# Kernel tuning notes

Hardware: AMD Instinct MI355X
Metric: run time of the kernel (lower is better)

## Reference

```python
import jax, jax.numpy as jnp
import numpy as np

N_UNI = 32; N_G = 4; N_PPG = 8
MAX_D = 100.0; MIN_D = 0.5
SOM_SIGMA = 2.0; G_STD = 2.5
ORIG = jnp.array([-25.6, -25.6, -2.0], jnp.float32); VS = 0.4
NZ = 16; GW = 128; GL = 128; DIM = 128
H_IMG = 352; W_IMG = 1216

def pe(x):
    # positional encoding: num_freqs=6, include_input -> 3 + 36 = 39 dims
    f = 2.0 ** jnp.arange(6, dtype=x.dtype)
    xf = x[..., None] * f  # (...,3,6)
    s = x.shape[:-1]
    return jnp.concatenate([x, jnp.sin(xf).reshape(s + (18,)), jnp.cos(xf).reshape(s + (18,))], axis=-1)

def resnet_fc(z, x, P):
    # pixelNeRF-style ResnetFC with latent injection per block
    w_in, b_in, wz, bz, w0, b0, w1, b1, w_out, b_out = P
    h = x @ w_in + b_in
    for i in range(3):
        h = h + z @ wz[i] + bz[i]
        net = jax.nn.relu(h) @ w0[i] + b0[i]
        h = h + jax.nn.relu(net) @ w1[i] + b1[i]
    return jax.nn.relu(h) @ w_out + b_out

def trilinear(grid, pts):
    # grid: (NZ,GW,GL,DIM); pts: (N,3) lidar coords -> trilinear gather, 0 outside
    g = (pts - ORIG) / VS
    gx, gy, gz = g[:, 0], g[:, 1], g[:, 2]
    inb = (gx >= 0) & (gx <= GW - 1) & (gy >= 0) & (gy <= GL - 1) & (gz >= 0) & (gz <= NZ - 1)
    gx = jnp.clip(gx, 0.0, GW - 1.0); gy = jnp.clip(gy, 0.0, GL - 1.0); gz = jnp.clip(gz, 0.0, NZ - 1.0)
    x0 = jnp.clip(jnp.floor(gx).astype(jnp.int32), 0, GW - 2)
    y0 = jnp.clip(jnp.floor(gy).astype(jnp.int32), 0, GL - 2)
    z0 = jnp.clip(jnp.floor(gz).astype(jnp.int32), 0, NZ - 2)
    fx = gx - x0; fy = gy - y0; fz = gz - z0
    def c(zi, xi, yi, w):
        return grid[zi, xi, yi] * w[:, None]
    feat = (c(z0, x0, y0, (1 - fz) * (1 - fx) * (1 - fy)) + c(z0, x0, y0 + 1, (1 - fz) * (1 - fx) * fy)
            + c(z0, x0 + 1, y0, (1 - fz) * fx * (1 - fy)) + c(z0, x0 + 1, y0 + 1, (1 - fz) * fx * fy)
            + c(z0 + 1, x0, y0, fz * (1 - fx) * (1 - fy)) + c(z0 + 1, x0, y0 + 1, fz * (1 - fx) * fy)
            + c(z0 + 1, x0 + 1, y0, fz * fx * (1 - fy)) + c(z0 + 1, x0 + 1, y0 + 1, fz * fx * fy))
    return feat * inb[:, None].astype(feat.dtype)

def bilinear(img, uv):
    # img: (3,H,W); uv: (N,2) (u=col, v=row) -> (N,3)
    _, H, W = img.shape
    u = jnp.clip(uv[:, 0], 0.0, W - 1.0); v = jnp.clip(uv[:, 1], 0.0, H - 1.0)
    u0 = jnp.clip(jnp.floor(u).astype(jnp.int32), 0, W - 2)
    v0 = jnp.clip(jnp.floor(v).astype(jnp.int32), 0, H - 2)
    fu = u - u0; fv = v - v0
    g = lambda vi, ui: img[:, vi, ui]
    out = (g(v0, u0) * ((1 - fv) * (1 - fu)) + g(v0, u0 + 1) * ((1 - fv) * fu)
           + g(v0 + 1, u0) * (fv * (1 - fu)) + g(v0 + 1, u0 + 1) * (fv * fu))
    return out.T

def _forward(bev_feature, cam_K, img_source, img_target, T_source2infer, T_source2target,
             gaussian_noise, Pm, Pg, sampled_pixels):
    R = sampled_pixels.shape[0]
    # (B, C, W, L) -> (n_z, W, L, dim)
    vf = bev_feature[0].reshape(NZ, DIM, GW, GL).transpose(0, 2, 3, 1)
    inv_K = jnp.linalg.inv(cam_K)
    pix = sampled_pixels.astype(jnp.float32)
    homog = jnp.concatenate([pix, jnp.ones((R, 1), jnp.float32)], axis=1)
    dirs = homog @ inv_K.T
    unit = dirs / jnp.linalg.norm(dirs, axis=1, keepdims=True)  # (R,3) cam frame
    Rsi = T_source2infer[:3, :3]; tsi = T_source2infer[:3, 3]
    viewdir = unit @ Rsi.T  # lidar frame

    # --- predict per-ray gaussian means/stds at coarse segment centers ---
    base = (jnp.arange(N_G, dtype=jnp.float32) + 0.5) * (MAX_D / N_G)
    pg = (unit[:, None, :] * base[None, :, None]).reshape(-1, 3) @ Rsi.T + tsi
    fg = trilinear(vf, pg)
    vdg = jnp.broadcast_to(viewdir[:, None, :], (R, N_G, 3)).reshape(-1, 3)
    og = resnet_fc(fg, jnp.concatenate([pe(pg), vdg], axis=1), Pg)  # (R*N_G,2)
    means = jnp.clip(base[None, :] + og[:, 0].reshape(R, N_G), MIN_D, MAX_D)
    stds = G_STD * jax.nn.sigmoid(og[:, 1].reshape(R, N_G)) + 0.1

    # --- sample points: uniform + gaussian, sorted along ray ---
    d_g = jnp.clip(means[:, :, None] + stds[:, :, None] * gaussian_noise, MIN_D, MAX_D).reshape(R, N_G * N_PPG)
    d_u = jnp.broadcast_to(jnp.linspace(MIN_D, MAX_D, N_UNI, dtype=jnp.float32)[None, :], (R, N_UNI))
    d = jnp.sort(jnp.concatenate([d_u, d_g], axis=1), axis=1)  # (R,64)
    P = d.shape[1]
    pl = (unit[:, None, :] * d[..., None]).reshape(-1, 3) @ Rsi.T + tsi
    fl = trilinear(vf, pl)
    vd = jnp.broadcast_to(viewdir[:, None, :], (R, P, 3)).reshape(-1, 3)
    out = resnet_fc(fl, jnp.concatenate([pe(pl), vd], axis=1), Pm).reshape(R, P, 4)
    sigma = jax.nn.softplus(out[..., 0]); rgb = jax.nn.sigmoid(out[..., 1:])

    # --- volume rendering ---
    deltas = jnp.concatenate([d[:, 1:] - d[:, :-1], jnp.full((R, 1), 1e10, jnp.float32)], axis=1)
    alpha = 1.0 - jnp.exp(-sigma * deltas)
    trans = jnp.cumprod(1.0 - alpha + 1e-10, axis=1)
    trans = jnp.concatenate([jnp.ones((R, 1), jnp.float32), trans[:, :-1]], axis=1)
    w = alpha * trans
    depth = (w * d).sum(axis=1)          # (R,)
    color = (w[..., None] * rgb).sum(axis=1)  # (R,3)

    # --- losses ---
    diff = jnp.abs(means - jax.lax.stop_gradient(depth)[:, None])
    loss_dist = diff.min(axis=1)
    pdf = jnp.exp(-(d[:, None, :] - means[..., None]) ** 2 / (2.0 * stds[..., None] ** 2)) / (stds[..., None] * jnp.sqrt(2.0 * jnp.pi))
    loss_kl = (w * (-jnp.log(pdf.mean(axis=1) + 1e-6))).sum(axis=1)
    src = bilinear(img_source, pix)
    loss_color = jnp.abs(src - color)
    pcam = unit * depth[:, None]
    pt = pcam @ T_source2target[:3, :3].T + T_source2target[:3, 3]
    proj = pt @ cam_K.T
    uv = proj[:, :2] / jnp.clip(proj[:, 2:3], 1e-3)
    tgt = bilinear(img_target, uv)
    loss_reproj = jnp.abs(src - tgt)
    total = loss_reproj.mean() + loss_color.mean() + loss_kl.mean() + 0.01 * loss_dist.mean()
    return total

def setup_inputs() -> dict:
    key = jax.random.key(0)
    def rn(i, shape, s=1.0):
        return jax.random.normal(jax.random.fold_in(key, i), shape, jnp.float32) * s
    R = 4096
    inp = {}
    inp['bev_feature'] = rn(0, (1, NZ * DIM, GW, GL), 0.5)
    inp['cam_K'] = jnp.array([[720.0, 0.0, 608.0], [0.0, 720.0, 176.0], [0.0, 0.0, 1.0]], jnp.float32)
    inp['img_source'] = jax.random.uniform(jax.random.fold_in(key, 1), (3, H_IMG, W_IMG), jnp.float32)
    inp['img_target'] = jax.random.uniform(jax.random.fold_in(key, 2), (3, H_IMG, W_IMG), jnp.float32)
    Rcl = jnp.array([[0.0, 0.0, 1.0], [-1.0, 0.0, 0.0], [0.0, -1.0, 0.0]], jnp.float32)  # cam->lidar axes
    inp['T_source2infer'] = jnp.eye(4, dtype=jnp.float32).at[:3, :3].set(Rcl).at[:3, 3].set(jnp.array([0.5, 0.2, 0.1], jnp.float32))
    inp['T_source2target'] = jnp.eye(4, dtype=jnp.float32).at[0, 3].set(0.8).at[1, 3].set(0.05)
    inp['gaussian_noise'] = rn(3, (R, N_G, N_PPG))
    u = jax.random.randint(jax.random.fold_in(key, 4), (R,), 0, W_IMG)
    v = jax.random.randint(jax.random.fold_in(key, 5), (R,), 0, H_IMG)
    inp['sampled_pixels'] = jnp.stack([u, v], axis=1).astype(jnp.int32)
    for pfx, (i0, d_out) in {'m': (10, 4), 'g': (40, 2)}.items():
        inp[pfx + '_w_in'] = rn(i0, (42, 128), 0.05)
        inp[pfx + '_b_in'] = jnp.zeros((128,), jnp.float32)
        inp[pfx + '_wz'] = rn(i0 + 1, (3, 128, 128), 0.05)
        inp[pfx + '_bz'] = jnp.zeros((3, 128), jnp.float32)
        inp[pfx + '_w0'] = rn(i0 + 2, (3, 128, 128), 0.05)
        inp[pfx + '_b0'] = jnp.zeros((3, 128), jnp.float32)
        inp[pfx + '_w1'] = rn(i0 + 3, (3, 128, 128), 0.05)
        inp[pfx + '_b1'] = jnp.zeros((3, 128), jnp.float32)
        inp[pfx + '_w_out'] = rn(i0 + 4, (128, d_out), 0.05)
        inp[pfx + '_b_out'] = jnp.zeros((d_out,), jnp.float32)
    return inp

def reference(bev_feature, cam_K, img_source, img_target, T_source2infer, T_source2target,
              gaussian_noise, sampled_pixels,
              m_w_in, m_b_in, m_wz, m_bz, m_w0, m_b0, m_w1, m_b1, m_w_out, m_b_out,
              g_w_in, g_b_in, g_wz, g_bz, g_w0, g_b0, g_w1, g_b1, g_w_out, g_b_out):
    Pm = (m_w_in, m_b_in, m_wz, m_bz, m_w0, m_b0, m_w1, m_b1, m_w_out, m_b_out)
    Pg = (g_w_in, g_b_in, g_wz, g_bz, g_w0, g_b0, g_w1, g_b1, g_w_out, g_b_out)
    return _forward(bev_feature, cam_K, img_source, img_target, T_source2infer, T_source2target,
                    gaussian_noise, Pm, Pg, sampled_pixels)
```

## Files before the change

kernel.cpp:

```cpp
#include <hip/hip_runtime.h>

typedef __attribute__((ext_vector_type(8))) short short8;
typedef __attribute__((ext_vector_type(4))) float f32x4;
typedef __attribute__((ext_vector_type(2))) float f32x2;
typedef __attribute__((ext_vector_type(2))) unsigned u32x2;
typedef unsigned short ushort_t;

#define WIMG 1216
#define HIMG 352

__device__ __forceinline__ float sigmoid_(float x){ return 1.f/(1.f+__expf(-x)); }
__device__ __forceinline__ float softplus_(float x){
  return fmaxf(x,0.f) + log1pf(__expf(-fabsf(x)));
}
__device__ __forceinline__ ushort_t f2b(float x){
  union { float f; unsigned u; } v; v.f = x;
  unsigned r = v.u + 0x7FFF + ((v.u >> 16) & 1);
  return (ushort_t)(r >> 16);
}
__device__ __forceinline__ unsigned pack_trunc(float a, float b){
  union { float f; unsigned u; } va, vb; va.f = a; vb.f = b;
  return (va.u >> 16) | (vb.u & 0xFFFF0000u);
}
__device__ __forceinline__ unsigned cvt_pk_bf16(float a, float b){
  unsigned r;
  asm("v_cvt_pk_bf16_f32 %0, %1, %2" : "=v"(r) : "v"(a), "v"(b));
  return r;
}
__device__ __forceinline__ f32x2 bf2x(unsigned u){
  union { unsigned uu[2]; f32x2 f; } v;
  v.uu[0] = u << 16; v.uu[1] = u & 0xFFFF0000u;
  return v.f;
}

__global__ __launch_bounds__(256)
void k_prep(const float* __restrict__ bev, ushort_t* __restrict__ vfh, int mode,
            const float* __restrict__ mw_in, const float* __restrict__ mwz,
            const float* __restrict__ mw0, const float* __restrict__ mw1,
            const float* __restrict__ mwo,
            const float* __restrict__ gw_in, const float* __restrict__ gwz,
            const float* __restrict__ gw0, const float* __restrict__ gw1,
            const float* __restrict__ gwo,
            ushort_t* __restrict__ pkM, ushort_t* __restrict__ pkG,
            float* __restrict__ out0){
  int bx = blockIdx.x;
  int tid = threadIdx.x;
  if (bx < 8192) {
    if (!mode) return;
    __shared__ float tile[64][65];
    int y0 = (bx & 1) * 64;
    int c0 = ((bx >> 1) & 1) * 64;
    int zx = bx >> 2;
    const float* s = bev + (size_t)(zx >> 7)*2097152 + (size_t)c0*16384 + (size_t)(zx & 127)*128 + y0;
    int r0 = tid >> 4, f4 = tid & 15;
    #pragma unroll
    for (int it = 0; it < 4; ++it) {
      int c = it*16 + r0;
      f32x4 v = __builtin_nontemporal_load((const f32x4*)(s + (size_t)c*16384 + f4*4));
      tile[c][f4*4+0]=v.x; tile[c][f4*4+1]=v.y; tile[c][f4*4+2]=v.z; tile[c][f4*4+3]=v.w;
    }
    __syncthreads();
    ushort_t* d = vfh + ((size_t)zx*128 + y0)*128 + c0;
    #pragma unroll
    for (int it = 0; it < 4; ++it) {
      int y = it*16 + r0;
      u32x2 o;
      o.x = pack_trunc(tile[f4*4+0][y], tile[f4*4+1][y]);
      o.y = pack_trunc(tile[f4*4+2][y], tile[f4*4+3][y]);
      __builtin_nontemporal_store(o, (u32x2*)(d + (size_t)y*128 + f4*4));
    }
    return;
  }
  int pb = bx - 8192;
  if (pb == 0 && tid == 0) out0[0] = 0.f;
  int net = pb >= 624;
  const float* w_in = net ? gw_in : mw_in;
  const float* wz   = net ? gwz   : mwz;
  const float* w0   = net ? gw0   : mw0;
  const float* w1   = net ? gw1   : mw1;
  const float* wo   = net ? gwo   : mwo;
  int outd = net ? 2 : 4;
  ushort_t* pk = net ? pkG : pkM;
  int id = (pb - (net ? 624 : 0))*256 + tid;
  if (id >= 39*4096) return;
  int blk = id >> 12;
  int e = id & 4095;
  float val = 0.f;
  if (blk < 38) {
    int nt = e >> 9, lane = (e >> 3) & 63, j = e & 7;
    int kloc = (lane >> 4)*8 + j;
    int n = nt*16 + (lane & 15);
    if (blk < 2) {
      int k = blk*32 + kloc;
      val = (k < 42) ? w_in[k*128 + n] : 0.f;
    } else {
      int g = blk - 2;
      int i = g / 12, r = g % 12, m = r >> 2, ks = r & 3;
      int k = ks*32 + kloc;
      const float* src = (m==0 ? wz : (m==1 ? w0 : w1)) + i*16384;
      val = src[k*128 + n];
    }
  } else if (e < 2048) {
    int ks = e >> 9, lane = (e >> 3) & 63, j = e & 7;
    int k = ks*32 + (lane >> 4)*8 + j;
    int n = lane & 15;
    val = (n < outd) ? wo[k*outd + n] : 0.f;
  }
  pk[id] = f2b(val);
}

template<int KS, bool SWZ>
__device__ __forceinline__ void gemm_frag(const ushort_t* lds,
                                          const ushort_t* __restrict__ pkW,
                                          f32x4 acc[2][4], int wave, int lane)
{
  short8 w[KS][2];
  #pragma unroll
  for (int ks = 0; ks < KS; ++ks)
    #pragma unroll
    for (int ct = 0; ct < 2; ++ct)
      w[ks][ct] = *(const short8*)(pkW + (size_t)((ks*8 + wave*2 + ct)*64 + lane)*8);
  #pragma unroll
  for (int ks = 0; ks < KS; ++ks) {
    int idx = SWZ ? ((lane & ~7) | ((lane ^ (lane >> 3) ^ ks) & 7)) : lane;
    short8 b[4];
    #pragma unroll
    for (int nt = 0; nt < 4; ++nt)
      b[nt] = *(const short8*)(lds + (ks*4 + nt)*512 + idx*8);
    __builtin_amdgcn_s_setprio(1);
    #pragma unroll
    for (int ct = 0; ct < 2; ++ct)
      #pragma unroll
      for (int nt = 0; nt < 4; ++nt)
        acc[ct][nt] = __builtin_amdgcn_mfma_f32_16x16x32_bf16(w[ks][ct], b[nt], acc[ct][nt], 0,0,0);
    __builtin_amdgcn_s_setprio(0);
  }
}

__device__ __forceinline__ void store_reluF(ushort_t* buf, const f32x4 acc[2][4],
                                            int wave, int lane){
  int l15 = lane & 15, quad = lane >> 4;
  int j = (quad & 1)*4;
  #pragma unroll
  for (int ct = 0; ct < 2; ++ct) {
    int lp = (ct*2 + (quad >> 1))*16 + l15;
    #pragma unroll
    for (int nt = 0; nt < 4; ++nt) {
      uint2 o;
      o.x = cvt_pk_bf16(fmaxf(acc[ct][nt][0],0.f), fmaxf(acc[ct][nt][1],0.f));
      o.y = cvt_pk_bf16(fmaxf(acc[ct][nt][2],0.f), fmaxf(acc[ct][nt][3],0.f));
      *(uint2*)(buf + (wave*4 + nt)*512 + lp*8 + j) = o;
    }
  }
}

template<int OUTD>
__global__ __launch_bounds__(256, 4)
void k_fused(const ushort_t* __restrict__ vfh, const float* __restrict__ vf0, int mode,
             const float* __restrict__ camK, const int* __restrict__ pix,
             const float* __restrict__ noise,
             float* __restrict__ unit, float* __restrict__ viewdir,
             const float* __restrict__ Tsi, float* __restrict__ dsort,
             const ushort_t* __restrict__ pk,
             const float* __restrict__ b_in, const float* __restrict__ bzv,
             const float* __restrict__ b0v, const float* __restrict__ b1v,
             const float* __restrict__ b_out,
             float* __restrict__ means, float* __restrict__ stds, float* __restrict__ outbuf)
{
  __shared__ int   sOff[64];
  __shared__ float sW[64][8];
  __shared__ float sPx[64], sPy[64], sPz[64];
  __shared__ float sUx[16], sUy[16], sUz[16], sVx[16], sVy[16], sVz[16];
  __shared__ float sMean[64], sStd[64];
  __shared__ __align__(16) ushort_t zf[16*512];
  __shared__ __align__(16) ushort_t Wb[16*512];

  int tid = threadIdx.x;
  int qbase = blockIdx.x * 64;

  if constexpr (OUTD == 2) {
    if (tid < 16) {
      int gray = (qbase >> 2) + tid;
      float a=camK[0],b=camK[1],c=camK[2],d=camK[3],e=camK[4],f=camK[5],g=camK[6],h=camK[7],i=camK[8];
      float c00 = e*i-f*h, c01 = c*h-b*i, c02 = b*f-c*e;
      float c10 = f*g-d*i, c11 = a*i-c*g, c12 = c*d-a*f;
      float c20 = d*h-e*g, c21 = b*g-a*h, c22 = a*e-b*d;
      float det = a*c00 + b*c10 + c*c20;
      float id = 1.f/det;
      float u = (float)pix[2*gray], v = (float)pix[2*gray+1];
      float dx = (c00*u + c01*v + c02)*id;
      float dy = (c10*u + c11*v + c12)*id;
      float dz = (c20*u + c21*v + c22)*id;
      float n = sqrtf(dx*dx+dy*dy+dz*dz);
      dx/=n; dy/=n; dz/=n;
      sUx[tid]=dx; sUy[tid]=dy; sUz[tid]=dz;
      unit[3*gray]=dx; unit[3*gray+1]=dy; unit[3*gray+2]=dz;
      float vx = Tsi[0]*dx + Tsi[1]*dy + Tsi[2]*dz;
      float vy = Tsi[4]*dx + Tsi[5]*dy + Tsi[6]*dz;
      float vz = Tsi[8]*dx + Tsi[9]*dy + Tsi[10]*dz;
      sVx[tid]=vx; sVy[tid]=vy; sVz[tid]=vz;
      viewdir[3*gray]=vx; viewdir[3*gray+1]=vy; viewdir[3*gray+2]=vz;
    }
  } else {
    if (tid == 0) {
      int ray = blockIdx.x;
      sUx[0]=unit[3*ray]; sUy[0]=unit[3*ray+1]; sUz[0]=unit[3*ray+2];
      sVx[0]=viewdir[3*ray]; sVy[0]=viewdir[3*ray+1]; sVz[0]=viewdir[3*ray+2];
    }
  }
  __syncthreads();

  if (tid < 64) {
    float t, ux, uy, uz;
    if constexpr (OUTD == 2) {
      t = ((float)(tid & 3) + 0.5f) * 25.f;
      int lr = tid >> 2;
      ux = sUx[lr]; uy = sUy[lr]; uz = sUz[lr];
    } else {
      t = dsort[qbase + tid];
      ux = sUx[0]; uy = sUy[0]; uz = sUz[0];
    }
    float wx=ux*t, wy=uy*t, wz=uz*t;
    float px = Tsi[0]*wx + Tsi[1]*wy + Tsi[2]*wz + Tsi[3];
    float py = Tsi[4]*wx + Tsi[5]*wy + Tsi[6]*wz + Tsi[7];
    float pz = Tsi[8]*wx + Tsi[9]*wy + Tsi[10]*wz + Tsi[11];
    sPx[tid]=px; sPy[tid]=py; sPz[tid]=pz;
    float gx = (px + 25.6f)*2.5f;
    float gy = (py + 25.6f)*2.5f;
    float gz = (pz + 2.0f)*2.5f;
    bool inb = (gx>=0.f)&&(gx<=127.f)&&(gy>=0.f)&&(gy<=127.f)&&(gz>=0.f)&&(gz<=15.f);
    gx = fminf(fmaxf(gx,0.f),127.f);
    gy = fminf(fmaxf(gy,0.f),127.f);
    gz = fminf(fmaxf(gz,0.f),15.f);
    int x0 = min(max((int)floorf(gx),0),126);
    int y0 = min(max((int)floorf(gy),0),126);
    int z0 = min(max((int)floorf(gz),0),14);
    float fx = gx-(float)x0, fy = gy-(float)y0, fz = gz-(float)z0;
    float sc = inb ? 1.f : 0.f;
    float ax0 = 1.f-fx, ay0 = 1.f-fy;
    float az0 = (1.f-fz)*sc, az1 = fz*sc;
    float q00 = ax0*ay0, q01 = ax0*fy, q10 = fx*ay0, q11 = fx*fy;
    sW[tid][0] = az0*q00; sW[tid][1] = az0*q01; sW[tid][2] = az0*q10; sW[tid][3] = az0*q11;
    sW[tid][4] = az1*q00; sW[tid][5] = az1*q01; sW[tid][6] = az1*q10; sW[tid][7] = az1*q11;
    sOff[tid] = mode ? (((z0*128 + x0)*128 + y0)*128)
                     : (z0*2097152 + x0*128 + y0);
  }
  __syncthreads();

  for (int it = 0; it < 4; ++it) {
    int lin = it*256 + tid;
    int p = lin >> 4, cb = lin & 15;
    float4 wA = *(const float4*)&sW[p][0];
    float4 wB = *(const float4*)&sW[p][4];
    f32x2 r01={0.f,0.f}, r23={0.f,0.f}, r45={0.f,0.f}, r67={0.f,0.f};
    if (mode) {
      const ushort_t* b = vfh + sOff[p] + cb*8;
      uint4 v;
      #define ACC8(PTR, W) \
        v = *(const uint4*)(PTR); \
        r01 += (W)*bf2x(v.x); r23 += (W)*bf2x(v.y); \
        r45 += (W)*bf2x(v.z); r67 += (W)*bf2x(v.w);
      ACC8(b,                     wA.x)
      ACC8(b + 128,               wA.y)
      ACC8(b + 16384,             wA.z)
      ACC8(b + 16384 + 128,       wA.w)
      ACC8(b + 2097152,           wB.x)
      ACC8(b + 2097152 + 128,     wB.y)
      ACC8(b + 2097152 + 16384,   wB.z)
      ACC8(b + 2097152 + 16512,   wB.w)
      #undef ACC8
    } else {
      const float* bsrc = vf0 + sOff[p];
      float rr[8];
      #pragma unroll
      for (int k = 0; k < 8; ++k) {
        const float* bc = bsrc + (size_t)(cb*8 + k)*16384;
        rr[k] = wA.x*bc[0] + wA.y*bc[1] + wA.z*bc[128] + wA.w*bc[129]
              + wB.x*bc[2097152] + wB.y*bc[2097153] + wB.z*bc[2097280] + wB.w*bc[2097281];
      }
      r01 = (f32x2){rr[0],rr[1]}; r23 = (f32x2){rr[2],rr[3]};
      r45 = (f32x2){rr[4],rr[5]}; r67 = (f32x2){rr[6],rr[7]};
    }
    uint4 o;
    o.x = cvt_pk_bf16(r01.x, r01.y); o.y = cvt_pk_bf16(r23.x, r23.y);
    o.z = cvt_pk_bf16(r45.x, r45.y); o.w = cvt_pk_bf16(r67.x, r67.y);
    int T = (cb >> 2)*4 + (p >> 4);
    int lanep = (cb & 3)*16 + (p & 15);
    int lsw = (lanep & ~7) | ((lanep ^ (lanep >> 3) ^ (cb >> 2)) & 7);
    *(uint4*)(zf + T*512 + lsw*8) = o;
  }

  {
    int p = tid & 63, wv = tid >> 6;
    float px = sPx[p], py = sPy[p], pz = sPz[p];
    int lr = (OUTD == 2) ? (p >> 2) : 0;
    float vx = sVx[lr], vy = sVy[lr], vz = sVz[lr];
    #pragma unroll
    for (int hf = 0; hf < 2; ++hf) {
      int g = hf*4 + wv;
      float vals[8];
      #pragma unroll
      for (int j = 0; j < 8; ++j) {
        int d = g*8 + j;
        float val = 0.f;
        if (d < 3)      val = (d==0)?px:((d==1)?py:pz);
        else if (d < 39) {
          int s = d - 3; bool isSin = (s < 18); if (!isSin) s -= 18;
          int axis = s/6, fi = s%6;
          float base = (axis==0)?px:((axis==1)?py:pz);
          float arg = base * (float)(1 << fi);
          val = isSin ? __sinf(arg) : __cosf(arg);
        } else if (d < 42) {
          val = (d==39)?vx:((d==40)?vy:vz);
        }
        vals[j] = val;
      }
      uint4 o;
      o.x = cvt_pk_bf16(vals[0], vals[1]);
      o.y = cvt_pk_bf16(vals[2], vals[3]);
      o.z = cvt_pk_bf16(vals[4], vals[5]);
      o.w = cvt_pk_bf16(vals[6], vals[7]);
      *(uint4*)(Wb + (g>>2)*2048 + (p>>4)*512 + ((g&3)*16 + (p&15))*8) = o;
    }
  }
  __syncthreads();

  int wave = tid >> 6, lane = tid & 63;
  int l15 = lane & 15, quad = lane >> 4;
  int cbase = wave*32 + quad*4;

  f32x4 h[2][4];
  #pragma unroll
  for (int ct = 0; ct < 2; ++ct) {
    f32x4 bi = *(const f32x4*)(b_in + cbase + ct*16);
    #pragma unroll
    for (int nt = 0; nt < 4; ++nt) h[ct][nt] = bi;
  }
  gemm_frag<2,false>(Wb, pk, h, wave, lane);

  const ushort_t* pkl = pk + 2*4096;
  #pragma unroll 1
  for (int i3 = 0; i3 < 3; ++i3) {
    gemm_frag<4,true>(zf, pkl + (size_t)(i3*12)*4096, h, wave, lane);
    #pragma unroll
    for (int ct = 0; ct < 2; ++ct) {
      f32x4 bz = *(const f32x4*)(bzv + i3*128 + cbase + ct*16);
      #pragma unroll
      for (int nt = 0; nt < 4; ++nt) h[ct][nt] += bz;
    }
    __syncthreads();
    store_reluF(Wb, h, wave, lane);
    __syncthreads();
    f32x4 net[2][4];
    #pragma unroll
    for (int ct = 0; ct < 2; ++ct) {
      f32x4 c0b = *(const f32x4*)(b0v + i3*128 + cbase + ct*16);
      #pragma unroll
      for (int nt = 0; nt < 4; ++nt) net[ct][nt] = c0b;
    }
    gemm_frag<4,false>(Wb, pkl + (size_t)(i3*12+4)*4096, net, wave, lane);
    __syncthreads();
    store_reluF(Wb, net, wave, lane);
    __syncthreads();
    gemm_frag<4,false>(Wb, pkl + (size_t)(i3*12+8)*4096, h, wave, lane);
    #pragma unroll
    for (int ct = 0; ct < 2; ++ct) {
      f32x4 o1b = *(const f32x4*)(b1v + i3*128 + cbase + ct*16);
      #pragma unroll
      for (int nt = 0; nt < 4; ++nt) h[ct][nt] += o1b;
    }
  }
  __syncthreads();
  store_reluF(Wb, h, wave, lane);
  __syncthreads();

  {
    const ushort_t* pkw = pk + 38*4096;
    f32x4 oa = (f32x4){0.f,0.f,0.f,0.f};
    #pragma unroll
    for (int ks = 0; ks < 4; ++ks) {
      short8 w = *(const short8*)(pkw + (size_t)(ks*64 + lane)*8);
      short8 b = *(const short8*)(Wb + (ks*4 + wave)*512 + lane*8);
      oa = __builtin_amdgcn_mfma_f32_16x16x32_bf16(w, b, oa, 0,0,0);
    }
    if (quad == 0) {
      int lq = wave*16 + l15;
      int q = qbase + lq;
      if constexpr (OUTD == 4) {
        float4 o = { oa[0] + b_out[0], oa[1] + b_out[1], oa[2] + b_out[2], oa[3] + b_out[3] };
        *(float4*)(outbuf + (size_t)q*4) = o;
      } else {
        int g = q & 3;
        float m = fminf(fmaxf(((float)g + 0.5f)*25.f + oa[0] + b_out[0], 0.5f), 100.f);
        float sd = 2.5f*sigmoid_(oa[1] + b_out[1]) + 0.1f;
        means[q] = m; stds[q] = sd;
        sMean[lq] = m; sStd[lq] = sd;
      }
    }
  }

  if constexpr (OUTD == 2) {
    __syncthreads();
    float* fbuf = (float*)zf;
    int lr = tid >> 4;
    int sbase = (tid & 15) * 4;
    float vals[4];
    #pragma unroll
    for (int t = 0; t < 4; ++t) {
      int slot = sbase + t;
      float val;
      if (slot < 32) val = 0.5f + (float)slot * (99.5f/31.f);
      else {
        int idx = slot - 32, g = idx >> 3, s = idx & 7;
        int lq = lr*4 + g;
        float mu = sMean[lq], sd = sStd[lq];
        val = fminf(fmaxf(mu + sd*noise[(size_t)(qbase + lq)*8 + s], 0.5f), 100.f);
      }
      fbuf[lr*64 + slot] = val;
      vals[t] = val;
    }
    __syncthreads();
    int rk[4] = {0,0,0,0};
    for (int k = 0; k < 64; ++k) {
      float o = fbuf[lr*64 + k];
      #pragma unroll
      for (int t = 0; t < 4; ++t)
        rk[t] += (o < vals[t]) || (o == vals[t] && k < sbase + t);
    }
    int gray = (qbase >> 2) + lr;
    #pragma unroll
    for (int t = 0; t < 4; ++t)
      dsort[(size_t)gray*64 + rk[t]] = vals[t];
  }
}

__device__ __forceinline__ void bilin3(const float* __restrict__ img, float u, float v, float* out){
  u = fminf(fmaxf(u, 0.f), (float)(WIMG-1));
  v = fminf(fmaxf(v, 0.f), (float)(HIMG-1));
  int u0 = min(max((int)floorf(u),0), WIMG-2);
  int v0 = min(max((int)floorf(v),0), HIMG-2);
  float fu = u - (float)u0, fv = v - (float)v0;
  float w00=(1.f-fv)*(1.f-fu), w01=(1.f-fv)*fu, w10=fv*(1.f-fu), w11=fv*fu;
  #pragma unroll
  for (int c = 0; c < 3; ++c) {
    const float* b = img + (size_t)c*(HIMG*WIMG) + (size_t)v0*WIMG + u0;
    out[c] = w00*b[0] + w01*b[1] + w10*b[WIMG] + w11*b[WIMG+1];
  }
}

__global__ void k_render(const float* __restrict__ outbuf, const float* __restrict__ dsort,
                         const float* __restrict__ means, const float* __restrict__ stds,
                         const float* __restrict__ unit,
                         const float* __restrict__ img_src, const float* __restrict__ img_tgt,
                         const int* __restrict__ pix, const float* __restrict__ camK,
                         const float* __restrict__ Tst, float* __restrict__ loss_out, int R){
  __shared__ float accw[4];
  int gid = blockIdx.x*blockDim.x + threadIdx.x;
  int r = gid >> 6, lane = gid & 63;
  float d = dsort[(size_t)r*64 + lane];
  float dn = __shfl_down(d, 1);
  float delta = (lane < 63) ? (dn - d) : 1e10f;
  float4 o = *(const float4*)(outbuf + (size_t)r*256 + lane*4);
  float sig = softplus_(o.x);
  float alpha = 1.f - __expf(-sig*delta);
  float om = 1.f - alpha + 1e-10f;
  float prod = om;
  #pragma unroll
  for (int off = 1; off < 64; off <<= 1) {
    float v = __shfl_up(prod, off);
    if (lane >= off) prod *= v;
  }
  float texc = __shfl_up(prod, 1);
  if (lane == 0) texc = 1.f;
  float w = alpha * texc;
  float m0=means[r*4],m1=means[r*4+1],m2=means[r*4+2],m3=means[r*4+3];
  float s0=stds[r*4], s1=stds[r*4+1], s2=stds[r*4+2], s3=stds[r*4+3];
  float t0=(d-m0)/s0, t1=(d-m1)/s1, t2=(d-m2)/s2, t3=(d-m3)/s3;
  float pm = 0.25f*0.3989422804014327f*(__expf(-0.5f*t0*t0)/s0 + __expf(-0.5f*t1*t1)/s1
                                      + __expf(-0.5f*t2*t2)/s2 + __expf(-0.5f*t3*t3)/s3);
  float kl  = w * (-__logf(pm + 1e-6f));
  float dep = w * d;
  float c0 = w * sigmoid_(o.y);
  float c1 = w * sigmoid_(o.z);
  float c2 = w * sigmoid_(o.w);
  #pragma unroll
  for (int off = 32; off; off >>= 1) {
    dep += __shfl_xor(dep, off);
    c0  += __shfl_xor(c0, off);
    c1  += __shfl_xor(c1, off);
    c2  += __shfl_xor(c2, off);
    kl  += __shfl_xor(kl, off);
  }
  if (lane == 0) {
    float ld = fminf(fminf(fabsf(m0-dep),fabsf(m1-dep)), fminf(fabsf(m2-dep),fabsf(m3-dep)));
    float src[3], tgt[3];
    float u = (float)pix[2*r], v = (float)pix[2*r+1];
    bilin3(img_src, u, v, src);
    float ux=unit[3*r],uy=unit[3*r+1],uz=unit[3*r+2];
    float pcx=ux*dep, pcy=uy*dep, pcz=uz*dep;
    float ptx = Tst[0]*pcx + Tst[1]*pcy + Tst[2]*pcz + Tst[3];
    float pty = Tst[4]*pcx + Tst[5]*pcy + Tst[6]*pcz + Tst[7];
    float ptz = Tst[8]*pcx + Tst[9]*pcy + Tst[10]*pcz + Tst[11];
    float prx = camK[0]*ptx + camK[1]*pty + camK[2]*ptz;
    float pry = camK[3]*ptx + camK[4]*pty + camK[5]*ptz;
    float prz = camK[6]*ptx + camK[7]*pty + camK[8]*ptz;
    prz = fmaxf(prz, 0.001f);
    bilin3(img_tgt, prx/prz, pry/prz, tgt);
    float lrepr = fabsf(src[0]-tgt[0])+fabsf(src[1]-tgt[1])+fabsf(src[2]-tgt[2]);
    float lcol  = fabsf(src[0]-c0)+fabsf(src[1]-c1)+fabsf(src[2]-c2);
    float invR = 1.f/(float)R;
    accw[threadIdx.x >> 6] = (lrepr + lcol) * (invR/3.f) + kl*invR + 0.01f*ld*invR;
  }
  __syncthreads();
  if (threadIdx.x == 0)
    atomicAdd(loss_out, accw[0]+accw[1]+accw[2]+accw[3]);
}

extern "C" void kernel_launch(void* const* d_in, const int* in_sizes, int n_in,
                              void* d_out, int out_size, void* d_ws, size_t ws_size,
                              hipStream_t stream)
{
  const float* bev   = (const float*)d_in[0];
  const float* camK  = (const float*)d_in[1];
  const float* img_s = (const float*)d_in[2];
  const float* img_t = (const float*)d_in[3];
  const float* Tsi   = (const float*)d_in[4];
  const float* Tst   = (const float*)d_in[5];
  const float* noise = (const float*)d_in[6];
  const int*   pix   = (const int*)d_in[7];
  const float* m_w_in=(const float*)d_in[8];  const float* m_b_in=(const float*)d_in[9];
  const float* m_wz  =(const float*)d_in[10]; const float* m_bz  =(const float*)d_in[11];
  const float* m_w0  =(const float*)d_in[12]; const float* m_b0  =(const float*)d_in[13];
  const float* m_w1  =(const float*)d_in[14]; const float* m_b1  =(const float*)d_in[15];
  const float* m_wo  =(const float*)d_in[16]; const float* m_bo  =(const float*)d_in[17];
  const float* g_w_in=(const float*)d_in[18]; const float* g_b_in=(const float*)d_in[19];
  const float* g_wz  =(const float*)d_in[20]; const float* g_bz  =(const float*)d_in[21];
  const float* g_w0  =(const float*)d_in[22]; const float* g_b0  =(const float*)d_in[23];
  const float* g_w1  =(const float*)d_in[24]; const float* g_b1  =(const float*)d_in[25];
  const float* g_wo  =(const float*)d_in[26]; const float* g_bo  =(const float*)d_in[27];

  int R = in_sizes[7] / 2;
  float* ws = (float*)d_ws;
  size_t off = 0;
  float* unitb = ws + off; off += (size_t)R*3;
  float* vdirb = ws + off; off += (size_t)R*3;
  float* means = ws + off; off += (size_t)R*4;
  float* stds  = ws + off; off += (size_t)R*4;
  float* dsort = ws + off; off += (size_t)R*64;
  float* outbf = ws + off; off += (size_t)R*256;
  ushort_t* pkM = (ushort_t*)(ws + off);
  ushort_t* pkG = pkM + 39*4096;
  off += 39*4096 + 64;
  off = (off + 63) & ~(size_t)63;
  ushort_t* vfh = (ushort_t*)(ws + off);
  size_t need = off*4ull + (size_t)16*128*128*128*2ull;
  int mode = (ws_size >= need) ? 1 : 0;

  k_prep<<<9440,256,0,stream>>>(bev, vfh, mode,
      m_w_in,m_wz,m_w0,m_w1,m_wo, g_w_in,g_wz,g_w0,g_w1,g_wo,
      pkM, pkG, (float*)d_out);
  k_fused<2><<<R/16,256,0,stream>>>(vfh,bev,mode,camK,pix,noise,unitb,vdirb,Tsi,dsort,pkG,
      g_b_in,g_bz,g_b0,g_b1,g_bo, means,stds,nullptr);
  k_fused<4><<<R,256,0,stream>>>(vfh,bev,mode,camK,pix,noise,unitb,vdirb,Tsi,dsort,pkM,
      m_b_in,m_bz,m_b0,m_b1,m_bo, means,stds,outbf);
  k_render<<<R/4,256,0,stream>>>(outbf,dsort,means,stds,unitb,img_s,img_t,pix,camK,Tst,
                                 (float*)d_out,R);
}
```

Measured before the change: 429.7 us.

## Replace shared-memory setup with per-wave redundant compute and lane shuffles in fused MLP kernel

Every wave now computes the ray direction, sample point and trilinear weights and offsets for its own 64 lanes in registers. Within the gather loop, the per-point weights and offsets are broadcast with __shfl instead of being read from shared arrays. This removes two __syncthreads barriers and several small shared arrays. Shared memory becomes dynamic and sized per instantiation, and the launch bound is raised to 5 blocks per SM to allow more occupancy. The cost is redundant per-wave address math and extra shuffle instructions, plus possible register pressure under the tighter launch bound.

```diff
diff --git a/kernel.cpp b/kernel.cpp
--- a/kernel.cpp
+++ b/kernel.cpp
@@ -155,7 +155,7 @@
 }
 
 template<int OUTD>
-__global__ __launch_bounds__(256, 4)
+__global__ __launch_bounds__(256, 5)
 void k_fused(const ushort_t* __restrict__ vfh, const float* __restrict__ vf0, int mode,
              const float* __restrict__ camK, const int* __restrict__ pix,
              const float* __restrict__ noise,
@@ -167,64 +167,54 @@
              const float* __restrict__ b_out,
              float* __restrict__ means, float* __restrict__ stds, float* __restrict__ outbuf)
 {
-  __shared__ int   sOff[64];
-  __shared__ float sW[64][8];
-  __shared__ float sPx[64], sPy[64], sPz[64];
-  __shared__ float sUx[16], sUy[16], sUz[16], sVx[16], sVy[16], sVz[16];
-  __shared__ float sMean[64], sStd[64];
-  __shared__ __align__(16) ushort_t zf[16*512];
-  __shared__ __align__(16) ushort_t Wb[16*512];
+  extern __shared__ ushort_t smem[];
+  ushort_t* zf = smem;
+  ushort_t* Wb = smem + 8192;
+  float* sMean = (float*)(smem + 16384);
+  float* sStd  = sMean + 64;
 
   int tid = threadIdx.x;
+  int wave = tid >> 6, lane = tid & 63;
   int qbase = blockIdx.x * 64;
 
-  if constexpr (OUTD == 2) {
-    if (tid < 16) {
-      int gray = (qbase >> 2) + tid;
+  float vx, vy, vz, t, px, py, pz;
+  float4 wA, wB;
+  int off;
+  {
+    float ux, uy, uz;
+    if constexpr (OUTD == 2) {
+      int gray = (qbase >> 2) + (lane >> 2);
       float a=camK[0],b=camK[1],c=camK[2],d=camK[3],e=camK[4],f=camK[5],g=camK[6],h=camK[7],i=camK[8];
       float c00 = e*i-f*h, c01 = c*h-b*i, c02 = b*f-c*e;
       float c10 = f*g-d*i, c11 = a*i-c*g, c12 = c*d-a*f;
       float c20 = d*h-e*g, c21 = b*g-a*h, c22 = a*e-b*d;
       float det = a*c00 + b*c10 + c*c20;
-      float id = 1.f/det;
+      float idt = 1.f/det;
       float u = (float)pix[2*gray], v = (float)pix[2*gray+1];
-      float dx = (c00*u + c01*v + c02)*id;
-      float dy = (c10*u + c11*v + c12)*id;
-      float dz = (c20*u + c21*v + c22)*id;
+      float dx = (c00*u + c01*v + c02)*idt;
+      float dy = (c10*u + c11*v + c12)*idt;
+      float dz = (c20*u + c21*v + c22)*idt;
       float n = sqrtf(dx*dx+dy*dy+dz*dz);
       dx/=n; dy/=n; dz/=n;
-      sUx[tid]=dx; sUy[tid]=dy; sUz[tid]=dz;
-      unit[3*gray]=dx; unit[3*gray+1]=dy; unit[3*gray+2]=dz;
-      float vx = Tsi[0]*dx + Tsi[1]*dy + Tsi[2]*dz;
-      float vy = Tsi[4]*dx + Tsi[5]*dy + Tsi[6]*dz;
-      float vz = Tsi[8]*dx + Tsi[9]*dy + Tsi[10]*dz;
-      sVx[tid]=vx; sVy[tid]=vy; sVz[tid]=vz;
-      viewdir[3*gray]=vx; viewdir[3*gray+1]=vy; viewdir[3*gray+2]=vz;
-    }
-  } else {
-    if (tid == 0) {
+      ux=dx; uy=dy; uz=dz;
+      vx = Tsi[0]*dx + Tsi[1]*dy + Tsi[2]*dz;
+      vy = Tsi[4]*dx + Tsi[5]*dy + Tsi[6]*dz;
+      vz = Tsi[8]*dx + Tsi[9]*dy + Tsi[10]*dz;
+      if (wave == 0 && (lane & 3) == 0) {
+        unit[3*gray]=ux; unit[3*gray+1]=uy; unit[3*gray+2]=uz;
+        viewdir[3*gray]=vx; viewdir[3*gray+1]=vy; viewdir[3*gray+2]=vz;
+      }
+      t = ((float)(lane & 3) + 0.5f) * 25.f;
+    } else {
       int ray = blockIdx.x;
-      sUx[0]=unit[3*ray]; sUy[0]=unit[3*ray+1]; sUz[0]=unit[3*ray+2];
-      sVx[0]=viewdir[3*ray]; sVy[0]=viewdir[3*ray+1]; sVz[0]=viewdir[3*ray+2];
-    }
-  }
-  __syncthreads();
-
-  if (tid < 64) {
-    float t, ux, uy, uz;
-    if constexpr (OUTD == 2) {
-      t = ((float)(tid & 3) + 0.5f) * 25.f;
-      int lr = tid >> 2;
-      ux = sUx[lr]; uy = sUy[lr]; uz = sUz[lr];
-    } else {
-      t = dsort[qbase + tid];
-      ux = sUx[0]; uy = sUy[0]; uz = sUz[0];
+      ux = unit[3*ray]; uy = unit[3*ray+1]; uz = unit[3*ray+2];
+      vx = viewdir[3*ray]; vy = viewdir[3*ray+1]; vz = viewdir[3*ray+2];
+      t = dsort[qbase + lane];
     }
     float wx=ux*t, wy=uy*t, wz=uz*t;
-    float px = Tsi[0]*wx + Tsi[1]*wy + Tsi[2]*wz + Tsi[3];
-    float py = Tsi[4]*wx + Tsi[5]*wy + Tsi[6]*wz + Tsi[7];
-    float pz = Tsi[8]*wx + Tsi[9]*wy + Tsi[10]*wz + Tsi[11];
-    sPx[tid]=px; sPy[tid]=py; sPz[tid]=pz;
+    px = Tsi[0]*wx + Tsi[1]*wy + Tsi[2]*wz + Tsi[3];
+    py = Tsi[4]*wx + Tsi[5]*wy + Tsi[6]*wz + Tsi[7];
+    pz = Tsi[8]*wx + Tsi[9]*wy + Tsi[10]*wz + Tsi[11];
     float gx = (px + 25.6f)*2.5f;
     float gy = (py + 25.6f)*2.5f;
     float gz = (pz + 2.0f)*2.5f;
@@ -240,43 +230,46 @@
     float ax0 = 1.f-fx, ay0 = 1.f-fy;
     float az0 = (1.f-fz)*sc, az1 = fz*sc;
     float q00 = ax0*ay0, q01 = ax0*fy, q10 = fx*ay0, q11 = fx*fy;
-    sW[tid][0] = az0*q00; sW[tid][1] = az0*q01; sW[tid][2] = az0*q10; sW[tid][3] = az0*q11;
-    sW[tid][4] = az1*q00; sW[tid][5] = az1*q01; sW[tid][6] = az1*q10; sW[tid][7] = az1*q11;
-    sOff[tid] = mode ? (((z0*128 + x0)*128 + y0)*128)
-                     : (z0*2097152 + x0*128 + y0);
-  }
-  __syncthreads();
+    wA = make_float4(az0*q00, az0*q01, az0*q10, az0*q11);
+    wB = make_float4(az1*q00, az1*q01, az1*q10, az1*q11);
+    off = mode ? (((z0*128 + x0)*128 + y0)*128)
+               : (z0*2097152 + x0*128 + y0);
+  }
 
   for (int it = 0; it < 4; ++it) {
-    int lin = it*256 + tid;
-    int p = lin >> 4, cb = lin & 15;
-    float4 wA = *(const float4*)&sW[p][0];
-    float4 wB = *(const float4*)&sW[p][4];
+    int psrc = it*16 + wave*4 + (lane >> 4);
+    float4 swA, swB;
+    swA.x = __shfl(wA.x, psrc); swA.y = __shfl(wA.y, psrc);
+    swA.z = __shfl(wA.z, psrc); swA.w = __shfl(wA.w, psrc);
+    swB.x = __shfl(wB.x, psrc); swB.y = __shfl(wB.y, psrc);
+    swB.z = __shfl(wB.z, psrc); swB.w = __shfl(wB.w, psrc);
+    int soff = __shfl(off, psrc);
+    int cb = lane & 15;
     f32x2 r01={0.f,0.f}, r23={0.f,0.f}, r45={0.f,0.f}, r67={0.f,0.f};
     if (mode) {
-      const ushort_t* b = vfh + sOff[p] + cb*8;
+      const ushort_t* b = vfh + soff + cb*8;
       uint4 v;
       #define ACC8(PTR, W) \
         v = *(const uint4*)(PTR); \
         r01 += (W)*bf2x(v.x); r23 += (W)*bf2x(v.y); \
         r45 += (W)*bf2x(v.z); r67 += (W)*bf2x(v.w);
-      ACC8(b,                     wA.x)
-      ACC8(b + 128,               wA.y)
-      ACC8(b + 16384,             wA.z)
-      ACC8(b + 16384 + 128,       wA.w)
-      ACC8(b + 2097152,           wB.x)
-      ACC8(b + 2097152 + 128,     wB.y)
-      ACC8(b + 2097152 + 16384,   wB.z)
-      ACC8(b + 2097152 + 16512,   wB.w)
+      ACC8(b,                     swA.x)
+      ACC8(b + 128,               swA.y)
+      ACC8(b + 16384,             swA.z)
+      ACC8(b + 16384 + 128,       swA.w)
+      ACC8(b + 2097152,           swB.x)
+      ACC8(b + 2097152 + 128,     swB.y)
+      ACC8(b + 2097152 + 16384,   swB.z)
+      ACC8(b + 2097152 + 16512,   swB.w)
       #undef ACC8
     } else {
-      const float* bsrc = vf0 + sOff[p];
+      const float* bsrc = vf0 + soff;
       float rr[8];
       #pragma unroll
       for (int k = 0; k < 8; ++k) {
         const float* bc = bsrc + (size_t)(cb*8 + k)*16384;
-        rr[k] = wA.x*bc[0] + wA.y*bc[1] + wA.z*bc[128] + wA.w*bc[129]
-              + wB.x*bc[2097152] + wB.y*bc[2097153] + wB.z*bc[2097280] + wB.w*bc[2097281];
+        rr[k] = swA.x*bc[0] + swA.y*bc[1] + swA.z*bc[128] + swA.w*bc[129]
+              + swB.x*bc[2097152] + swB.y*bc[2097153] + swB.z*bc[2097280] + swB.w*bc[2097281];
       }
       r01 = (f32x2){rr[0],rr[1]}; r23 = (f32x2){rr[2],rr[3]};
       r45 = (f32x2){rr[4],rr[5]}; r67 = (f32x2){rr[6],rr[7]};
@@ -284,20 +277,17 @@
     uint4 o;
     o.x = cvt_pk_bf16(r01.x, r01.y); o.y = cvt_pk_bf16(r23.x, r23.y);
     o.z = cvt_pk_bf16(r45.x, r45.y); o.w = cvt_pk_bf16(r67.x, r67.y);
-    int T = (cb >> 2)*4 + (p >> 4);
-    int lanep = (cb & 3)*16 + (p & 15);
+    int T = (cb >> 2)*4 + it;
+    int lanep = (cb & 3)*16 + (psrc & 15);
     int lsw = (lanep & ~7) | ((lanep ^ (lanep >> 3) ^ (cb >> 2)) & 7);
     *(uint4*)(zf + T*512 + lsw*8) = o;
   }
 
   {
-    int p = tid & 63, wv = tid >> 6;
-    float px = sPx[p], py = sPy[p], pz = sPz[p];
-    int lr = (OUTD == 2) ? (p >> 2) : 0;
-    float vx = sVx[lr], vy = sVy[lr], vz = sVz[lr];
+    int p = lane;
     #pragma unroll
     for (int hf = 0; hf < 2; ++hf) {
-      int g = hf*4 + wv;
+      int g = hf*4 + wave;
       float vals[8];
       #pragma unroll
       for (int j = 0; j < 8; ++j) {
@@ -325,7 +315,6 @@
   }
   __syncthreads();
 
-  int wave = tid >> 6, lane = tid & 63;
   int l15 = lane & 15, quad = lane >> 4;
   int cbase = wave*32 + quad*4;
 
@@ -406,31 +395,31 @@
     int sbase = (tid & 15) * 4;
     float vals[4];
     #pragma unroll
-    for (int t = 0; t < 4; ++t) {
-      int slot = sbase + t;
+    for (int s = 0; s < 4; ++s) {
+      int slot = sbase + s;
       float val;
       if (slot < 32) val = 0.5f + (float)slot * (99.5f/31.f);
       else {
-        int idx = slot - 32, g = idx >> 3, s = idx & 7;
+        int idx = slot - 32, g = idx >> 3, sx = idx & 7;
         int lq = lr*4 + g;
         float mu = sMean[lq], sd = sStd[lq];
-        val = fminf(fmaxf(mu + sd*noise[(size_t)(qbase + lq)*8 + s], 0.5f), 100.f);
+        val = fminf(fmaxf(mu + sd*noise[(size_t)(qbase + lq)*8 + sx], 0.5f), 100.f);
       }
       fbuf[lr*64 + slot] = val;
-      vals[t] = val;
+      vals[s] = val;
     }
     __syncthreads();
     int rk[4] = {0,0,0,0};
     for (int k = 0; k < 64; ++k) {
       float o = fbuf[lr*64 + k];
       #pragma unroll
-      for (int t = 0; t < 4; ++t)
-        rk[t] += (o < vals[t]) || (o == vals[t] && k < sbase + t);
+      for (int s = 0; s < 4; ++s)
+        rk[s] += (o < vals[s]) || (o == vals[s] && k < sbase + s);
     }
     int gray = (qbase >> 2) + lr;
     #pragma unroll
-    for (int t = 0; t < 4; ++t)
-      dsort[(size_t)gray*64 + rk[t]] = vals[t];
+    for (int s = 0; s < 4; ++s)
+      dsort[(size_t)gray*64 + rk[s]] = vals[s];
   }
 }
 
@@ -559,9 +548,9 @@
   k_prep<<<9440,256,0,stream>>>(bev, vfh, mode,
       m_w_in,m_wz,m_w0,m_w1,m_wo, g_w_in,g_wz,g_w0,g_w1,g_wo,
       pkM, pkG, (float*)d_out);
-  k_fused<2><<<R/16,256,0,stream>>>(vfh,bev,mode,camK,pix,noise,unitb,vdirb,Tsi,dsort,pkG,
+  k_fused<2><<<R/16,256, 2*16384 + 512, stream>>>(vfh,bev,mode,camK,pix,noise,unitb,vdirb,Tsi,dsort,pkG,
       g_b_in,g_bz,g_b0,g_b1,g_bo, means,stds,nullptr);
-  k_fused<4><<<R,256,0,stream>>>(vfh,bev,mode,camK,pix,noise,unitb,vdirb,Tsi,dsort,pkM,
+  k_fused<4><<<R,256, 2*16384, stream>>>(vfh,bev,mode,camK,pix,noise,unitb,vdirb,Tsi,dsort,pkM,
       m_b_in,m_bz,m_b0,m_b1,m_bo, means,stds,outbf);
   k_render<<<R/4,256,0,stream>>>(outbf,dsort,means,stds,unitb,img_s,img_t,pix,camK,Tst,
                                  (float*)d_out,R);
```

Measured after the change: 564.2 us. 1.31x slower.
